# Performance work log

Measured on AMD Instinct MI355X. Metric: run time of the kernel, lower is better.

Reference implementation:

```python
import jax, jax.numpy as jnp
import numpy as np

IN_SIZE, HID_SIZE, OUT_SIZE = 256, 512, 256
BATCH, NSTEPS = 64, 2048


def setup_inputs() -> dict:
    key = jax.random.key(0)
    ks = jax.random.split(key, 6)
    s_ih = 1.0 / np.sqrt(IN_SIZE)
    s_hh = 1.0 / np.sqrt(HID_SIZE)
    return {
        "input": jax.random.normal(ks[0], (BATCH, NSTEPS, IN_SIZE), dtype=jnp.float32),
        "w_ih": jax.random.uniform(ks[1], (HID_SIZE, IN_SIZE), jnp.float32, -s_ih, s_ih),
        "w_hh": jax.random.uniform(ks[2], (HID_SIZE, HID_SIZE), jnp.float32, -s_hh, s_hh),
        "b_h": jax.random.uniform(ks[3], (HID_SIZE,), jnp.float32, -s_hh, s_hh),
        "w_out": jax.random.uniform(ks[4], (OUT_SIZE, HID_SIZE), jnp.float32, -s_hh, s_hh),
        "b_out": jax.random.uniform(ks[5], (OUT_SIZE,), jnp.float32, -s_hh, s_hh),
    }


def reference(input, w_ih, w_hh, b_h, w_out, b_out):
    # Vanilla RNN recurrence (delay=1 in the original forward) + linear readout.
    # h_t = tanh(x_t W_ih^T + h_{t-1} W_hh^T + b_h);  y_t = h_t W_out^T + b_out
    batch = input.shape[0]
    h0 = jnp.zeros((batch, w_hh.shape[0]), dtype=input.dtype)
    # Precompute input projections for all steps in one big GEMM (same math).
    x_proj = jnp.einsum("bti,hi->bth", input, w_ih) + b_h  # [B, T, H]

    def step(h, xp_t):
        h_new = jnp.tanh(xp_t + h @ w_hh.T)
        return h_new, h_new

    _, hs = jax.lax.scan(step, h0, jnp.swapaxes(x_proj, 0, 1))  # hs: [T, B, H]
    hs = jnp.swapaxes(hs, 0, 1)  # [B, T, H]
    outputs = jnp.einsum("bth,oh->bto", hs, w_out) + b_out  # [B, T, O]
    return outputs
```

## Files before the change

### kernel.cpp

```cpp
#include <hip/hip_runtime.h>


typedef _Float16 f16;
typedef __attribute__((ext_vector_type(2))) _Float16 half2_t;
typedef __attribute__((ext_vector_type(4))) float float4_t;

#define NIN    256
#define NHID   512
#define NOUT   256
#define NBATCH 64
#define NT     2048

#define FL4(p) (*reinterpret_cast<const float4_t*>(p))
#define LOADA(p)     __hip_atomic_load((p), __ATOMIC_RELAXED, __HIP_MEMORY_SCOPE_AGENT)
#define STOREA(p, v) __hip_atomic_store((p), (v), __ATOMIC_RELAXED, __HIP_MEMORY_SCOPE_AGENT)

#if __has_builtin(__builtin_amdgcn_fdot2)
__device__ __forceinline__ float fdot2f(half2_t a, half2_t b, float c) {
  return __builtin_amdgcn_fdot2(a, b, c, false);
}
#else
__device__ __forceinline__ float fdot2f(half2_t a, half2_t b, float c) {
  return c + (float)a.x * (float)b.x + (float)a.y * (float)b.y;
}
#endif

__device__ float g_hpub[NBATCH][2][NHID];
__device__ __align__(64) int g_flag[NBATCH * 64];

__global__ __launch_bounds__(256) void k_zero() {
  g_flag[blockIdx.x * 256 + threadIdx.x] = 0;
}

__global__ __launch_bounds__(256) void k_inproj(
    const float* __restrict__ x, const float* __restrict__ w,
    const float* __restrict__ bias, float* __restrict__ xplo, float* __restrict__ xphi)
{
  __shared__ float xs[32][260];
  __shared__ float wsT[8][520];
  const int t = threadIdx.x;
  const int m0 = blockIdx.x * 32;
  const int mthr = t & 3;
  const int nthr = t >> 2;

  #pragma unroll
  for (int r = 0; r < 8; ++r) {
    int f = (t + 256 * r) * 4;
    int row = f >> 8, col = f & 255;
    *(float4_t*)&xs[row][col] =
        *reinterpret_cast<const float4_t*>(x + (size_t)(m0 + row) * NIN + col);
  }

  float acc[8][8];
  #pragma unroll
  for (int nn = 0; nn < 8; ++nn) {
    float bv = bias[nthr * 8 + nn];
    #pragma unroll
    for (int mm = 0; mm < 8; ++mm) acc[nn][mm] = bv;
  }

  for (int kc = 0; kc < 32; ++kc) {
    __syncthreads();
    #pragma unroll
    for (int r = 0; r < 4; ++r) {
      int f = (t + 256 * r) * 4;
      int n = f >> 3, k0 = f & 7;
      float4_t v = *reinterpret_cast<const float4_t*>(w + (size_t)n * NIN + kc * 8 + k0);
      #pragma unroll
      for (int j = 0; j < 4; ++j) wsT[k0 + j][n] = v[j];
    }
    __syncthreads();
    #pragma unroll
    for (int kp = 0; kp < 8; ++kp) {
      float4_t wv0 = *(const float4_t*)&wsT[kp][nthr * 8];
      float4_t wv1 = *(const float4_t*)&wsT[kp][nthr * 8 + 4];
      #pragma unroll
      for (int mm = 0; mm < 8; ++mm) {
        float xv = xs[mthr * 8 + mm][kc * 8 + kp];
        acc[0][mm] = fmaf(wv0.x, xv, acc[0][mm]);
        acc[1][mm] = fmaf(wv0.y, xv, acc[1][mm]);
        acc[2][mm] = fmaf(wv0.z, xv, acc[2][mm]);
        acc[3][mm] = fmaf(wv0.w, xv, acc[3][mm]);
        acc[4][mm] = fmaf(wv1.x, xv, acc[4][mm]);
        acc[5][mm] = fmaf(wv1.y, xv, acc[5][mm]);
        acc[6][mm] = fmaf(wv1.z, xv, acc[6][mm]);
        acc[7][mm] = fmaf(wv1.w, xv, acc[7][mm]);
      }
    }
  }

  const int n0 = nthr * 8;
  float* dst = (n0 < 256) ? (xplo + n0) : (xphi + (n0 - 256));
  #pragma unroll
  for (int mm = 0; mm < 8; ++mm) {
    int m = m0 + mthr * 8 + mm;
    float4_t o0 = {acc[0][mm], acc[1][mm], acc[2][mm], acc[3][mm]};
    float4_t o1 = {acc[4][mm], acc[5][mm], acc[6][mm], acc[7][mm]};
    *reinterpret_cast<float4_t*>(dst + (size_t)m * 256)     = o0;
    *reinterpret_cast<float4_t*>(dst + (size_t)m * 256 + 4) = o1;
  }
}

__global__ __launch_bounds__(512, 1) void k_recur(
    const float* __restrict__ whh, float* outbuf, float* wsbuf)
{
  __shared__ __align__(16) float hb[2][NHID];
  __shared__ __align__(16) float pacc[8][128];
  const int g = blockIdx.x;
  const int b = (g >> 5) * 8 + (g & 7);
  const int q = (g >> 3) & 3;
  const int t = threadIdx.x;
  const int js = t & 63;
  const int ks = t >> 6;
  const int r0 = q * 128 + js * 2, r1 = r0 + 1;
  const bool ownk = (ks >> 1) == q;

  float4_t w0[16], w1[16];
  #pragma unroll
  for (int i = 0; i < 16; ++i) {
    w0[i] = FL4(whh + (size_t)r0 * NHID + ks * 64 + i * 4);
    w1[i] = FL4(whh + (size_t)r1 * NHID + ks * 64 + i * 4);
  }

  float* xp = ((q < 2) ? (outbuf + q * 128) : (wsbuf + (q - 2) * 128))
              + (size_t)b * NT * 256 + t;
  float xq0 = 0.f, xq1 = 0.f;
  if (t < 128) { xq0 = xp[0]; xq1 = xp[256]; }

  hb[0][t] = 0.0f;
  __syncthreads();

  for (int s = 0; s < NT; ++s) {
    float* hbc = hb[s & 1];
    float* hbn = hb[(s & 1) ^ 1];

    float4_t a0 = {0.f,0.f,0.f,0.f}, a1 = {0.f,0.f,0.f,0.f};
    float4_t b0 = {0.f,0.f,0.f,0.f}, b1 = {0.f,0.f,0.f,0.f};

    if (ownk) {
      const float4_t* h4 = (const float4_t*)&hbc[ks * 64];
      #pragma unroll
      for (int i = 0; i < 16; i += 2) {
        float4_t hA = h4[i], hB = h4[i + 1];
        a0 += w0[i] * hA;  a1 += w0[i + 1] * hB;
        b0 += w1[i] * hA;  b1 += w1[i + 1] * hB;
      }
    }

    if (s > 0) {
      if (t < 3) {
        const int pq = (q + 1 + t) & 3;
        while (LOADA(&g_flag[b * 64 + pq * 16]) < s) {}
      }
      __syncthreads();
      if (t < 384) {
        const int prow = (q * 128 + 128 + t) & 511;
        hbc[prow] = LOADA(&g_hpub[b][(s - 1) & 1][prow]);
      }
      __syncthreads();
    }

    if (!ownk) {
      const float4_t* h4 = (const float4_t*)&hbc[ks * 64];
      #pragma unroll
      for (int i = 0; i < 16; i += 2) {
        float4_t hA = h4[i], hB = h4[i + 1];
        a0 += w0[i] * hA;  a1 += w0[i + 1] * hB;
        b0 += w1[i] * hA;  b1 += w1[i + 1] * hB;
      }
    }

    float4_t av = a0 + a1, bv = b0 + b1;
    pacc[ks][js * 2]     = (av.x + av.y) + (av.z + av.w);
    pacc[ks][js * 2 + 1] = (bv.x + bv.y) + (bv.z + bv.w);
    __syncthreads();

    if (t < 128) {
      float sum = pacc[0][t];
      #pragma unroll
      for (int k2 = 1; k2 < 8; ++k2) sum += pacc[k2][t];
      float h = tanhf(sum + xq0);
      hbn[q * 128 + t] = h;
      STOREA(&g_hpub[b][s & 1][q * 128 + t], h);
      xp[(size_t)s * 256] = h;
      xq0 = xq1;
      if (s + 2 < NT) xq1 = xp[(size_t)(s + 2) * 256];
    }
    __syncthreads();
    if (t == 0) STOREA(&g_flag[b * 64 + q * 16], s + 1);
  }
}

__global__ __launch_bounds__(256) void k_outproj(
    const float* hlo, const float* hhi, const float* __restrict__ w,
    const float* __restrict__ bias, float* out)
{
  __shared__ half2_t xs[32][258];
  __shared__ half2_t ws[256][19];
  const int t = threadIdx.x;
  const int m0 = blockIdx.x * 32;
  const int nthr = t >> 2;
  const int mthr = t & 3;

  #pragma unroll
  for (int r = 0; r < 16; ++r) {
    int f = (t + 256 * r) * 4;
    int row = f >> 9, col = f & 511;
    const float* src = (col < 256) ? (hlo + (size_t)(m0 + row) * 256 + col)
                                   : (hhi + (size_t)(m0 + row) * 256 + (col - 256));
    float4_t v = *reinterpret_cast<const float4_t*>(src);
    xs[row][(col >> 1)]     = half2_t{(f16)v.x, (f16)v.y};
    xs[row][(col >> 1) + 1] = half2_t{(f16)v.z, (f16)v.w};
  }

  float acc[4][8];
  #pragma unroll
  for (int nn = 0; nn < 4; ++nn) {
    float bv = bias[nthr * 4 + nn];
    #pragma unroll
    for (int mm = 0; mm < 8; ++mm) acc[nn][mm] = bv;
  }

  for (int kc = 0; kc < 16; ++kc) {
    __syncthreads();
    #pragma unroll
    for (int r = 0; r < 8; ++r) {
      int f = (t + 256 * r) * 4;
      int row = f >> 5, col = f & 31;
      float4_t v = *reinterpret_cast<const float4_t*>(w + (size_t)row * NHID + kc * 32 + col);
      ws[row][(col >> 1)]     = half2_t{(f16)v.x, (f16)v.y};
      ws[row][(col >> 1) + 1] = half2_t{(f16)v.z, (f16)v.w};
    }
    __syncthreads();
    #pragma unroll
    for (int kp = 0; kp < 16; ++kp) {
      half2_t wv[4], xv[8];
      #pragma unroll
      for (int nn = 0; nn < 4; ++nn) wv[nn] = ws[nthr * 4 + nn][kp];
      #pragma unroll
      for (int mm = 0; mm < 8; ++mm) xv[mm] = xs[mthr * 8 + mm][kc * 16 + kp];
      #pragma unroll
      for (int nn = 0; nn < 4; ++nn)
        #pragma unroll
        for (int mm = 0; mm < 8; ++mm)
          acc[nn][mm] = fdot2f(wv[nn], xv[mm], acc[nn][mm]);
    }
  }

  #pragma unroll
  for (int mm = 0; mm < 8; ++mm) {
    int m = m0 + mthr * 8 + mm;
    float4_t o = {acc[0][mm], acc[1][mm], acc[2][mm], acc[3][mm]};
    *reinterpret_cast<float4_t*>(out + (size_t)m * NOUT + nthr * 4) = o;
  }
}

extern "C" void kernel_launch(void* const* d_in, const int* in_sizes, int n_in,
                              void* d_out, int out_size, void* d_ws, size_t ws_size,
                              hipStream_t stream) {
  (void)in_sizes; (void)n_in; (void)ws_size; (void)out_size;
  const float* x     = (const float*)d_in[0];
  const float* w_ih  = (const float*)d_in[1];
  const float* w_hh  = (const float*)d_in[2];
  const float* b_h   = (const float*)d_in[3];
  const float* w_out = (const float*)d_in[4];
  const float* b_out = (const float*)d_in[5];

  float* outb = (float*)d_out;
  float* wsb  = (float*)d_ws;

  k_zero   <<<16, 256, 0, stream>>>();
  k_inproj <<<(NBATCH * NT) / 32, 256, 0, stream>>>(x, w_ih, b_h, outb, wsb);
  k_recur  <<<256, 512, 0, stream>>>(w_hh, outb, wsb);
  k_outproj<<<(NBATCH * NT) / 32, 256, 0, stream>>>(outb, wsb, w_out, b_out, outb);
}
```

Baseline: 4.675 ms.

## Interleave two batch recurrences per block to hide cross-block sync latency

Each recurrence block now handles two batch elements alternately, using separate shared h buffers, and the grid is halved from 256 to 128 blocks. While one batch waits on peer flags for its hidden-state exchange, the other batch's step can be issued, which should hide spin-wait and global-memory latency. In exchange each block does twice the serial work per step with more barriers, and half the CUs sit idle.

```diff
diff --git a/kernel.cpp b/kernel.cpp
--- a/kernel.cpp
+++ b/kernel.cpp
@@ -104,11 +104,13 @@
 __global__ __launch_bounds__(512, 1) void k_recur(
     const float* __restrict__ whh, float* outbuf, float* wsbuf)
 {
-  __shared__ __align__(16) float hb[2][NHID];
+  __shared__ __align__(16) float hbA[2][NHID];
+  __shared__ __align__(16) float hbB[2][NHID];
   __shared__ __align__(16) float pacc[8][128];
   const int g = blockIdx.x;
-  const int b = (g >> 5) * 8 + (g & 7);
   const int q = (g >> 3) & 3;
+  const int G = (g & 7) + 8 * (g >> 5);
+  const int bA = 2 * G, bB = 2 * G + 1;
   const int t = threadIdx.x;
   const int js = t & 63;
   const int ks = t >> 6;
@@ -122,73 +124,80 @@
     w1[i] = FL4(whh + (size_t)r1 * NHID + ks * 64 + i * 4);
   }
 
-  float* xp = ((q < 2) ? (outbuf + q * 128) : (wsbuf + (q - 2) * 128))
-              + (size_t)b * NT * 256 + t;
-  float xq0 = 0.f, xq1 = 0.f;
-  if (t < 128) { xq0 = xp[0]; xq1 = xp[256]; }
-
-  hb[0][t] = 0.0f;
+  float* xpA = ((q < 2) ? (outbuf + q * 128) : (wsbuf + (q - 2) * 128))
+               + (size_t)bA * NT * 256 + t;
+  float* xpB = ((q < 2) ? (outbuf + q * 128) : (wsbuf + (q - 2) * 128))
+               + (size_t)bB * NT * 256 + t;
+  float xqA0 = 0.f, xqA1 = 0.f, xqB0 = 0.f, xqB1 = 0.f;
+  if (t < 128) {
+    xqA0 = xpA[0]; xqA1 = xpA[256];
+    xqB0 = xpB[0]; xqB1 = xpB[256];
+  }
+
+  hbA[0][t] = 0.0f;
+  hbB[0][t] = 0.0f;
   __syncthreads();
 
+  #define SECTION(BB, HB, XP, XQ0, XQ1)                                          \
+  {                                                                              \
+    float* hbc = HB[s & 1];                                                      \
+    float* hbn = HB[(s & 1) ^ 1];                                                \
+    float4_t a0 = {0.f,0.f,0.f,0.f}, a1 = {0.f,0.f,0.f,0.f};                     \
+    float4_t b0 = {0.f,0.f,0.f,0.f}, b1 = {0.f,0.f,0.f,0.f};                     \
+    if (ownk) {                                                                  \
+      const float4_t* h4 = (const float4_t*)&hbc[ks * 64];                       \
+      _Pragma("unroll")                                                          \
+      for (int i = 0; i < 16; i += 2) {                                          \
+        float4_t hA = h4[i], hB = h4[i + 1];                                     \
+        a0 += w0[i] * hA;  a1 += w0[i + 1] * hB;                                 \
+        b0 += w1[i] * hA;  b1 += w1[i + 1] * hB;                                 \
+      }                                                                          \
+    }                                                                            \
+    if (s > 0) {                                                                 \
+      if (t < 3) {                                                               \
+        const int pq = (q + 1 + t) & 3;                                          \
+        while (LOADA(&g_flag[(BB) * 64 + pq * 16]) < s) {}                       \
+      }                                                                          \
+      __syncthreads();                                                           \
+      if (t < 384) {                                                             \
+        const int prow = (q * 128 + 128 + t) & 511;                              \
+        hbc[prow] = LOADA(&g_hpub[BB][(s - 1) & 1][prow]);                       \
+      }                                                                          \
+      __syncthreads();                                                           \
+    }                                                                            \
+    if (!ownk) {                                                                 \
+      const float4_t* h4 = (const float4_t*)&hbc[ks * 64];                       \
+      _Pragma("unroll")                                                          \
+      for (int i = 0; i < 16; i += 2) {                                          \
+        float4_t hA = h4[i], hB = h4[i + 1];                                     \
+        a0 += w0[i] * hA;  a1 += w0[i + 1] * hB;                                 \
+        b0 += w1[i] * hA;  b1 += w1[i + 1] * hB;                                 \
+      }                                                                          \
+    }                                                                            \
+    float4_t av = a0 + a1, bv = b0 + b1;                                         \
+    pacc[ks][js * 2]     = (av.x + av.y) + (av.z + av.w);                        \
+    pacc[ks][js * 2 + 1] = (bv.x + bv.y) + (bv.z + bv.w);                        \
+    __syncthreads();                                                             \
+    if (t < 128) {                                                               \
+      float sum = pacc[0][t];                                                    \
+      _Pragma("unroll")                                                          \
+      for (int k2 = 1; k2 < 8; ++k2) sum += pacc[k2][t];                         \
+      float h = tanhf(sum + XQ0);                                                \
+      hbn[q * 128 + t] = h;                                                      \
+      STOREA(&g_hpub[BB][s & 1][q * 128 + t], h);                                \
+      (XP)[(size_t)s * 256] = h;                                                 \
+      XQ0 = XQ1;                                                                 \
+      if (s + 2 < NT) XQ1 = (XP)[(size_t)(s + 2) * 256];                         \
+    }                                                                            \
+    __syncthreads();                                                             \
+    if (t == 0) STOREA(&g_flag[(BB) * 64 + q * 16], s + 1);                      \
+  }
+
   for (int s = 0; s < NT; ++s) {
-    float* hbc = hb[s & 1];
-    float* hbn = hb[(s & 1) ^ 1];
-
-    float4_t a0 = {0.f,0.f,0.f,0.f}, a1 = {0.f,0.f,0.f,0.f};
-    float4_t b0 = {0.f,0.f,0.f,0.f}, b1 = {0.f,0.f,0.f,0.f};
-
-    if (ownk) {
-      const float4_t* h4 = (const float4_t*)&hbc[ks * 64];
-      #pragma unroll
-      for (int i = 0; i < 16; i += 2) {
-        float4_t hA = h4[i], hB = h4[i + 1];
-        a0 += w0[i] * hA;  a1 += w0[i + 1] * hB;
-        b0 += w1[i] * hA;  b1 += w1[i + 1] * hB;
-      }
-    }
-
-    if (s > 0) {
-      if (t < 3) {
-        const int pq = (q + 1 + t) & 3;
-        while (LOADA(&g_flag[b * 64 + pq * 16]) < s) {}
-      }
-      __syncthreads();
-      if (t < 384) {
-        const int prow = (q * 128 + 128 + t) & 511;
-        hbc[prow] = LOADA(&g_hpub[b][(s - 1) & 1][prow]);
-      }
-      __syncthreads();
-    }
-
-    if (!ownk) {
-      const float4_t* h4 = (const float4_t*)&hbc[ks * 64];
-      #pragma unroll
-      for (int i = 0; i < 16; i += 2) {
-        float4_t hA = h4[i], hB = h4[i + 1];
-        a0 += w0[i] * hA;  a1 += w0[i + 1] * hB;
-        b0 += w1[i] * hA;  b1 += w1[i + 1] * hB;
-      }
-    }
-
-    float4_t av = a0 + a1, bv = b0 + b1;
-    pacc[ks][js * 2]     = (av.x + av.y) + (av.z + av.w);
-    pacc[ks][js * 2 + 1] = (bv.x + bv.y) + (bv.z + bv.w);
-    __syncthreads();
-
-    if (t < 128) {
-      float sum = pacc[0][t];
-      #pragma unroll
-      for (int k2 = 1; k2 < 8; ++k2) sum += pacc[k2][t];
-      float h = tanhf(sum + xq0);
-      hbn[q * 128 + t] = h;
-      STOREA(&g_hpub[b][s & 1][q * 128 + t], h);
-      xp[(size_t)s * 256] = h;
-      xq0 = xq1;
-      if (s + 2 < NT) xq1 = xp[(size_t)(s + 2) * 256];
-    }
-    __syncthreads();
-    if (t == 0) STOREA(&g_flag[b * 64 + q * 16], s + 1);
-  }
+    SECTION(bA, hbA, xpA, xqA0, xqA1)
+    SECTION(bB, hbB, xpB, xqB0, xqB1)
+  }
+  #undef SECTION
 }
 
 __global__ __launch_bounds__(256) void k_outproj(
@@ -271,6 +280,6 @@
 
   k_zero   <<<16, 256, 0, stream>>>();
   k_inproj <<<(NBATCH * NT) / 32, 256, 0, stream>>>(x, w_ih, b_h, outb, wsb);
-  k_recur  <<<256, 512, 0, stream>>>(w_hh, outb, wsb);
+  k_recur  <<<128, 512, 0, stream>>>(w_hh, outb, wsb);
   k_outproj<<<(NBATCH * NT) / 32, 256, 0, stream>>>(outb, wsb, w_out, b_out, outb);
 }
```

Result: slower. 7.829 ms (+67.5%).
